# Performance work log

Measured on AMD Instinct MI355X. Metric: run time of the kernel, lower is better.

The kernel has to match this reference:

```python
import jax, jax.numpy as jnp
import numpy as np

FIRE_RATE = 0.5
ANGLE = 0.0

def _sobel_kernels(angle=ANGLE):
    dx = np.outer([1, 2, 1], [-1, 0, 1]) / 8.0
    dy = dx.T
    c = np.cos(angle * np.pi / 180.0)
    s = np.sin(angle * np.pi / 180.0)
    w1 = (c * dx - s * dy).astype(np.float32)
    w2 = (s * dx + c * dy).astype(np.float32)
    # torch applies conv after transpose(1,3) so its spatial axes are (W,H);
    # transposing kernels makes our NHWC conv over (H,W) match exactly.
    return jnp.asarray(w1.T), jnp.asarray(w2.T)

def _depthwise3x3(x, w):
    # x: [B,H,W,C], w: [3,3] shared across all C channels (groups=C)
    C = x.shape[-1]
    k = jnp.tile(w[:, :, None, None], (1, 1, 1, C))  # [3,3,1,C] HWIO
    return jax.lax.conv_general_dilated(
        x, k, window_strides=(1, 1), padding='SAME',
        dimension_numbers=('NHWC', 'HWIO', 'NHWC'),
        feature_group_count=C)

def setup_inputs() -> dict:
    key = jax.random.key(0)
    k1, k2, k3 = jax.random.split(key, 3)
    B, H, W, C, HID = 8, 256, 256, 16, 128
    x = jax.random.uniform(k1, (B, H, W, C), dtype=jnp.float32)
    # xavier-uniform-like init for fc0/fc1
    lim0 = float(np.sqrt(6.0 / (3 * C + HID)))
    lim1 = float(np.sqrt(6.0 / (HID + C)))
    W0 = jax.random.uniform(k2, (HID, 3 * C), minval=-lim0, maxval=lim0, dtype=jnp.float32)
    b0 = jnp.zeros((HID,), dtype=jnp.float32)
    W1 = jax.random.uniform(k3, (C, HID), minval=-lim1, maxval=lim1, dtype=jnp.float32)
    return {'x': x, 'W0': W0, 'b0': b0, 'W1': W1, 'steps': 2}

def reference(x, W0, b0, W1, steps):
    w1, w2 = _sobel_kernels()
    key = jax.random.key(42)
    for step in range(steps):
        # perceive: identity + two depthwise sobel filters -> [B,H,W,3C]
        y = jnp.concatenate([x, _depthwise3x3(x, w1), _depthwise3x3(x, w2)], axis=-1)
        # per-cell MLP
        h = jax.nn.relu(jnp.einsum('bhwk,ok->bhwo', y, W0) + b0)
        dx = jnp.einsum('bhwo,co->bhwc', h, W1)
        # stochastic fire-rate mask [B,H,W,1]
        mk = jax.random.fold_in(key, step)
        mask = (jax.random.uniform(mk, dx.shape[:3] + (1,)) > FIRE_RATE).astype(dx.dtype)
        new = x + dx * mask
        # only channels 3: are updated (first 3 channels stay fixed)
        x = jnp.concatenate([x[..., :3], new[..., 3:]], axis=-1)
    return x
```

## Files before the change

kernel.cpp:

```cpp
#include <hip/hip_runtime.h>
#include <hip/hip_bf16.h>
#include <stdint.h>


#define NB 8
#define NH 256
#define NW 256
#define NC 16
#define TH 4
#define TW 16
#define WOFF 65536

typedef __attribute__((ext_vector_type(8))) short short8;
typedef __attribute__((ext_vector_type(4))) float floatx4;

__host__ __device__ inline void tf2x32(uint32_t k0, uint32_t k1,
                                       uint32_t x0, uint32_t x1,
                                       uint32_t& o0, uint32_t& o1) {
  const uint32_t ks2 = k0 ^ k1 ^ 0x1BD11BDAu;
  x0 += k0; x1 += k1;
#define RL(v, d) (((v) << (d)) | ((v) >> (32 - (d))))
#define R4(a, b, c, d)                          \
  x0 += x1; x1 = RL(x1, a); x1 ^= x0;           \
  x0 += x1; x1 = RL(x1, b); x1 ^= x0;           \
  x0 += x1; x1 = RL(x1, c); x1 ^= x0;           \
  x0 += x1; x1 = RL(x1, d); x1 ^= x0;
  R4(13, 15, 26, 6);  x0 += k1;  x1 += ks2 + 1u;
  R4(17, 29, 16, 24); x0 += ks2; x1 += k0 + 2u;
  R4(13, 15, 26, 6);  x0 += k0;  x1 += k1 + 3u;
  R4(17, 29, 16, 24); x0 += k1;  x1 += ks2 + 4u;
  R4(13, 15, 26, 6);  x0 += ks2; x1 += k0 + 5u;
#undef R4
#undef RL
  o0 = x0; o1 = x1;
}

__device__ inline short bfr(float x) {
  __hip_bfloat16 h = __float2bfloat16(x);
  return *reinterpret_cast<short*>(&h);
}

__global__ __launch_bounds__(64) void ca_prep(
    const float* __restrict__ W0, const float* __restrict__ b0,
    const float* __restrict__ W1, short* __restrict__ wbuf) {
  const int lane = threadIdx.x;
  const int c15 = lane & 15;
  const int g = lane >> 4;
  short8* wf = reinterpret_cast<short8*>(wbuf);

#pragma unroll
  for (int n = 0; n < 8; ++n) {
    const int o = 16 * n + c15;
    const float* p = W0 + o * 48 + 8 * g;
    const floatx4 v0 = *reinterpret_cast<const floatx4*>(p);
    const floatx4 v1 = *reinterpret_cast<const floatx4*>(p + 4);
    short8 f;
    f[0] = bfr(v0.x); f[1] = bfr(v0.y); f[2] = bfr(v0.z); f[3] = bfr(v0.w);
    f[4] = bfr(v1.x); f[5] = bfr(v1.y); f[6] = bfr(v1.z); f[7] = bfr(v1.w);
    wf[(2 * n) * 64 + lane] = f;
    short8 f1;
    if (g < 2) {
      const float* p1 = W0 + o * 48 + 32 + 8 * g;
      const floatx4 u0 = *reinterpret_cast<const floatx4*>(p1);
      const floatx4 u1 = *reinterpret_cast<const floatx4*>(p1 + 4);
      f1[0] = bfr(u0.x); f1[1] = bfr(u0.y); f1[2] = bfr(u0.z); f1[3] = bfr(u0.w);
      f1[4] = bfr(u1.x); f1[5] = bfr(u1.y); f1[6] = bfr(u1.z); f1[7] = bfr(u1.w);
    } else {
#pragma unroll
      for (int j = 0; j < 8; ++j) f1[j] = 0;
      if (g == 2) f1[0] = bfr(b0[o]);
    }
    wf[(2 * n + 1) * 64 + lane] = f1;
  }
#pragma unroll
  for (int s = 0; s < 4; ++s) {
    const float* p = W1 + c15 * 128 + 32 * s + 4 * g;
    const floatx4 v0 = *reinterpret_cast<const floatx4*>(p);
    const floatx4 v1 = *reinterpret_cast<const floatx4*>(p + 16);
    short8 f;
    f[0] = bfr(v0.x); f[1] = bfr(v0.y); f[2] = bfr(v0.z); f[3] = bfr(v0.w);
    f[4] = bfr(v1.x); f[5] = bfr(v1.y); f[6] = bfr(v1.z); f[7] = bfr(v1.w);
    wf[(16 + s) * 64 + lane] = f;
  }
}

template <bool PRE>
__global__ __launch_bounds__(64, 2) void ca_step(
    const float* __restrict__ xin, float* __restrict__ xout,
    const float* __restrict__ W0, const float* __restrict__ b0,
    const float* __restrict__ W1, const short* __restrict__ wfrag,
    uint32_t fk0, uint32_t fk1) {
  __shared__ float xs[2][6 * 18 * 16];

  const int tid = threadIdx.x;
  const int bt = blockIdx.x;
  const int wt = bt & 15;
  const int ht8 = (bt >> 4) & 31;
  const int b = bt >> 9;
  const int h0 = ht8 * 8;
  const int w0 = wt * TW;

  const int lane = tid;
  const int c15 = lane & 15;
  const int g = lane >> 4;

  auto xsaddr = [&](float* base, int row, int col, int chunk) -> floatx4* {
    const int off = (row * 18 + col) * 64 + ((chunk ^ ((col >> 1) & 3)) << 4);
    return reinterpret_cast<floatx4*>(reinterpret_cast<char*>(base) + off);
  };

  short8 w0f[8][2];
  short8 w1f[4];
  if constexpr (PRE) {
    const short8* wf = reinterpret_cast<const short8*>(wfrag);
#pragma unroll
    for (int n = 0; n < 8; ++n) {
      w0f[n][0] = wf[(2 * n) * 64 + lane];
      w0f[n][1] = wf[(2 * n + 1) * 64 + lane];
    }
#pragma unroll
    for (int s = 0; s < 4; ++s) w1f[s] = wf[(16 + s) * 64 + lane];
  } else {
#pragma unroll
    for (int n = 0; n < 8; ++n) {
      const int o = 16 * n + c15;
      const float* p = W0 + o * 48 + 8 * g;
      const floatx4 v0 = *reinterpret_cast<const floatx4*>(p);
      const floatx4 v1 = *reinterpret_cast<const floatx4*>(p + 4);
      short8 f;
      f[0] = bfr(v0.x); f[1] = bfr(v0.y); f[2] = bfr(v0.z); f[3] = bfr(v0.w);
      f[4] = bfr(v1.x); f[5] = bfr(v1.y); f[6] = bfr(v1.z); f[7] = bfr(v1.w);
      w0f[n][0] = f;
      short8 f1;
      if (g < 2) {
        const float* p1 = W0 + o * 48 + 32 + 8 * g;
        const floatx4 u0 = *reinterpret_cast<const floatx4*>(p1);
        const floatx4 u1 = *reinterpret_cast<const floatx4*>(p1 + 4);
        f1[0] = bfr(u0.x); f1[1] = bfr(u0.y); f1[2] = bfr(u0.z); f1[3] = bfr(u0.w);
        f1[4] = bfr(u1.x); f1[5] = bfr(u1.y); f1[6] = bfr(u1.z); f1[7] = bfr(u1.w);
      } else {
#pragma unroll
        for (int j = 0; j < 8; ++j) f1[j] = 0;
        if (g == 2) f1[0] = bfr(b0[o]);
      }
      w0f[n][1] = f1;
    }
#pragma unroll
    for (int s = 0; s < 4; ++s) {
      const float* p = W1 + c15 * 128 + 32 * s + 4 * g;
      const floatx4 v0 = *reinterpret_cast<const floatx4*>(p);
      const floatx4 v1 = *reinterpret_cast<const floatx4*>(p + 16);
      short8 f;
      f[0] = bfr(v0.x); f[1] = bfr(v0.y); f[2] = bfr(v0.z); f[3] = bfr(v0.w);
      f[4] = bfr(v1.x); f[5] = bfr(v1.y); f[6] = bfr(v1.z); f[7] = bfr(v1.w);
      w1f[s] = f;
    }
  }

  float wts[8];
  {
    const float Ac[3] = {1.f, 2.f, 1.f};
    const float Bc[3] = {-1.f, 0.f, 1.f};
    int t = 0;
#pragma unroll
    for (int dh = -1; dh <= 1; ++dh)
#pragma unroll
      for (int dw = -1; dw <= 1; ++dw) {
        if (dh == 0 && dw == 0) continue;
        const float wA = Ac[dw + 1] * Bc[dh + 1] * 0.125f;
        const float wB = Ac[dh + 1] * Bc[dw + 1] * 0.125f;
        wts[t++] = (g < 2) ? wB : wA;
      }
  }

  const int cc = 2 * (g & 1);

#pragma unroll 1
  for (int t2 = 0; t2 < 2; ++t2) {
    const int h0t = h0 + TH * t2;
    float* xsb = xs[t2];

    for (int f = tid; f < 6 * 18 * 4; f += 64) {
      const int row = f / 72;
      const int rem = f - row * 72;
      const int col = rem >> 2;
      const int q = rem & 3;
      const int gh = h0t - 1 + row;
      const int gw = w0 - 1 + col;
      floatx4 v = {0.f, 0.f, 0.f, 0.f};
      if ((unsigned)gh < (unsigned)NH && (unsigned)gw < (unsigned)NW)
        v = *reinterpret_cast<const floatx4*>(
            xin + (((size_t)b * NH + gh) * NW + gw) * NC + 4 * q);
      *xsaddr(xsb, row, col, q) = v;
    }

    uint64_t mball;
    {
      const int cellg = (b * NH + h0t + (lane >> 4)) * NW + w0 + c15;
      uint32_t r0, r1;
      tf2x32(fk0, fk1, 0u, (uint32_t)cellg, r0, r1);
      const uint32_t bits = r0 ^ r1;
      const float u = __uint_as_float((bits >> 9) | 0x3F800000u) - 1.0f;
      mball = __ballot(u > 0.5f);
    }
    __syncthreads();

#pragma unroll
    for (int mt = 0; mt < 4; ++mt) {
      const int r = 1 + mt;
      const int col = 1 + c15;

      const floatx4 xc0 = *xsaddr(xsb, r, col, cc);
      const floatx4 xc1 = *xsaddr(xsb, r, col, cc + 1);

      float sob[8];
#pragma unroll
      for (int j = 0; j < 8; ++j) sob[j] = 0.f;
      int t = 0;
#pragma unroll
      for (int dh = -1; dh <= 1; ++dh)
#pragma unroll
        for (int dw = -1; dw <= 1; ++dw) {
          if (dh == 0 && dw == 0) continue;
          const floatx4 v0 = *xsaddr(xsb, r + dh, col + dw, cc);
          const floatx4 v1 = *xsaddr(xsb, r + dh, col + dw, cc + 1);
          const float w = wts[t++];
          sob[0] += w * v0.x; sob[1] += w * v0.y;
          sob[2] += w * v0.z; sob[3] += w * v0.w;
          sob[4] += w * v1.x; sob[5] += w * v1.y;
          sob[6] += w * v1.z; sob[7] += w * v1.w;
        }

      const bool lo = (g < 2);
      const float xcv[8] = {xc0.x, xc0.y, xc0.z, xc0.w,
                            xc1.x, xc1.y, xc1.z, xc1.w};
      short8 a0, a1;
#pragma unroll
      for (int j = 0; j < 8; ++j) {
        const short sb = bfr(sob[j]);
        a0[j] = lo ? bfr(xcv[j]) : sb;
        a1[j] = lo ? sb : (short)0;
      }
      if (g == 2) a1[0] = bfr(1.0f);

      floatx4 acc[8];
#pragma unroll
      for (int n = 0; n < 8; ++n) acc[n] = floatx4{0.f, 0.f, 0.f, 0.f};
#pragma unroll
      for (int n = 0; n < 8; ++n)
        acc[n] = __builtin_amdgcn_mfma_f32_16x16x32_bf16(w0f[n][0], a0, acc[n], 0, 0, 0);
#pragma unroll
      for (int n = 0; n < 8; ++n)
        acc[n] = __builtin_amdgcn_mfma_f32_16x16x32_bf16(w0f[n][1], a1, acc[n], 0, 0, 0);

      floatx4 acc2 = {0.f, 0.f, 0.f, 0.f};
#pragma unroll
      for (int s = 0; s < 4; ++s) {
        short8 b2;
#pragma unroll
        for (int j = 0; j < 8; ++j)
          b2[j] = bfr(fmaxf(acc[2 * s + (j >> 2)][j & 3], 0.f));
        acc2 = __builtin_amdgcn_mfma_f32_16x16x32_bf16(w1f[s], b2, acc2, 0, 0, 0);
      }

      const floatx4 xv = *xsaddr(xsb, r, col, g);
      const float mk = (float)((mball >> (16 * mt + c15)) & 1ull);
      const float mk03 = (g == 0) ? 0.f : mk;
      floatx4 ov;
      ov.x = xv.x + acc2.x * mk03;
      ov.y = xv.y + acc2.y * mk03;
      ov.z = xv.z + acc2.z * mk03;
      ov.w = xv.w + acc2.w * mk;
      const size_t cellg = ((size_t)(b * NH + h0t + mt)) * NW + w0 + c15;
      *reinterpret_cast<floatx4*>(xout + cellg * NC + 4 * g) = ov;
    }
  }
}

extern "C" void kernel_launch(void* const* d_in, const int* in_sizes, int n_in,
                              void* d_out, int out_size, void* d_ws, size_t ws_size,
                              hipStream_t stream) {
  const float* x  = (const float*)d_in[0];
  const float* W0 = (const float*)d_in[1];
  const float* b0 = (const float*)d_in[2];
  const float* W1 = (const float*)d_in[3];
  float* out = (float*)d_out;

  const size_t tmp_bytes = (size_t)NB * NH * NW * NC * 4;
  const bool pre = ws_size >= (size_t)WOFF + tmp_bytes;
  short* wbuf = (short*)d_ws;
  float* tmp = pre ? (float*)((char*)d_ws + WOFF) : (float*)d_ws;

  uint32_t fa0, fa1, fb0, fb1;
  tf2x32(0u, 42u, 0u, 0u, fa0, fa1);
  tf2x32(0u, 42u, 0u, 1u, fb0, fb1);

  dim3 grid(NB * (NH / 8) * (NW / TW)), block(64);
  if (pre) {
    ca_prep<<<1, 64, 0, stream>>>(W0, b0, W1, wbuf);
    ca_step<true><<<grid, block, 0, stream>>>(x, tmp, W0, b0, W1, wbuf, fa0, fa1);
    ca_step<true><<<grid, block, 0, stream>>>(tmp, out, W0, b0, W1, wbuf, fb0, fb1);
  } else {
    ca_step<false><<<grid, block, 0, stream>>>(x, tmp, W0, b0, W1, nullptr, fa0, fa1);
    ca_step<false><<<grid, block, 0, stream>>>(tmp, out, W0, b0, W1, nullptr, fb0, fb1);
  }
}
```

Before: 70.66 us.

## Fold Sobel stencil into first-layer weights and compute via im2col MFMA

Folds the two fixed Sobel filters and the identity into an expanded first-layer weight matrix over the 3x3 neighbourhood (K=144 plus a bias chunk), so the per-cell stencil FMAs become extra MFMA K-steps that read bf16 neighbours straight from shared memory. The shared tile now holds bf16 instead of fp32, which halves LDS use and drops to a single buffer with an extra barrier. The residual x is reread from global memory in fp32. In exchange, first-layer MFMAs go from 16 to 40 per tile, weight registers grow from 16 to 40 short8 fragments, and the Sobel sums are no longer done in fp32 before rounding, which changes the numerics.

After: 130.8 us. 85.1% more time.

```diff
diff --git a/kernel.cpp b/kernel.cpp
--- a/kernel.cpp
+++ b/kernel.cpp
@@ -7,8 +7,6 @@
 #define NH 256
 #define NW 256
 #define NC 16
-#define TH 4
-#define TW 16
 #define WOFF 65536
 
 typedef __attribute__((ext_vector_type(8))) short short8;
@@ -40,6 +38,20 @@
   return *reinterpret_cast<short*>(&h);
 }
 
+__device__ inline float w0comp(const float* __restrict__ W0,
+                               const float* __restrict__ b0, int o, int k) {
+  const int t = k >> 4;
+  const int ch = k & 15;
+  if (t == 9) return (ch == 0) ? b0[o] : 0.f;
+  const int dh = t / 3 - 1, dw = t % 3 - 1;
+  const float Ac[3] = {1.f, 2.f, 1.f};
+  const float Bc[3] = {-1.f, 0.f, 1.f};
+  float v = (t == 4) ? W0[o * 48 + ch] : 0.f;
+  v += Ac[dw + 1] * Bc[dh + 1] * 0.125f * W0[o * 48 + 16 + ch];
+  v += Ac[dh + 1] * Bc[dw + 1] * 0.125f * W0[o * 48 + 32 + ch];
+  return v;
+}
+
 __global__ __launch_bounds__(64) void ca_prep(
     const float* __restrict__ W0, const float* __restrict__ b0,
     const float* __restrict__ W1, short* __restrict__ wbuf) {
@@ -48,39 +60,22 @@
   const int g = lane >> 4;
   short8* wf = reinterpret_cast<short8*>(wbuf);
 
-#pragma unroll
-  for (int n = 0; n < 8; ++n) {
-    const int o = 16 * n + c15;
-    const float* p = W0 + o * 48 + 8 * g;
-    const floatx4 v0 = *reinterpret_cast<const floatx4*>(p);
-    const floatx4 v1 = *reinterpret_cast<const floatx4*>(p + 4);
+  for (int n = 0; n < 8; ++n)
+    for (int q = 0; q < 5; ++q) {
+      short8 f;
+#pragma unroll
+      for (int j = 0; j < 8; ++j)
+        f[j] = bfr(w0comp(W0, b0, 16 * n + c15, 32 * q + 8 * g + j));
+      wf[(n * 5 + q) * 64 + lane] = f;
+    }
+#pragma unroll
+  for (int s = 0; s < 4; ++s) {
+    const float* p = W1 + c15 * 128;
     short8 f;
-    f[0] = bfr(v0.x); f[1] = bfr(v0.y); f[2] = bfr(v0.z); f[3] = bfr(v0.w);
-    f[4] = bfr(v1.x); f[5] = bfr(v1.y); f[6] = bfr(v1.z); f[7] = bfr(v1.w);
-    wf[(2 * n) * 64 + lane] = f;
-    short8 f1;
-    if (g < 2) {
-      const float* p1 = W0 + o * 48 + 32 + 8 * g;
-      const floatx4 u0 = *reinterpret_cast<const floatx4*>(p1);
-      const floatx4 u1 = *reinterpret_cast<const floatx4*>(p1 + 4);
-      f1[0] = bfr(u0.x); f1[1] = bfr(u0.y); f1[2] = bfr(u0.z); f1[3] = bfr(u0.w);
-      f1[4] = bfr(u1.x); f1[5] = bfr(u1.y); f1[6] = bfr(u1.z); f1[7] = bfr(u1.w);
-    } else {
-#pragma unroll
-      for (int j = 0; j < 8; ++j) f1[j] = 0;
-      if (g == 2) f1[0] = bfr(b0[o]);
-    }
-    wf[(2 * n + 1) * 64 + lane] = f1;
-  }
-#pragma unroll
-  for (int s = 0; s < 4; ++s) {
-    const float* p = W1 + c15 * 128 + 32 * s + 4 * g;
-    const floatx4 v0 = *reinterpret_cast<const floatx4*>(p);
-    const floatx4 v1 = *reinterpret_cast<const floatx4*>(p + 16);
-    short8 f;
-    f[0] = bfr(v0.x); f[1] = bfr(v0.y); f[2] = bfr(v0.z); f[3] = bfr(v0.w);
-    f[4] = bfr(v1.x); f[5] = bfr(v1.y); f[6] = bfr(v1.z); f[7] = bfr(v1.w);
-    wf[(16 + s) * 64 + lane] = f;
+#pragma unroll
+    for (int j = 0; j < 8; ++j)
+      f[j] = bfr(p[32 * s + 16 * (j >> 2) + 4 * g + (j & 3)]);
+    wf[(40 + s) * 64 + lane] = f;
   }
 }
 
@@ -90,7 +85,7 @@
     const float* __restrict__ W0, const float* __restrict__ b0,
     const float* __restrict__ W1, const short* __restrict__ wfrag,
     uint32_t fk0, uint32_t fk1) {
-  __shared__ float xs[2][6 * 18 * 16];
+  __shared__ __align__(16) uint16_t xs[6 * 18 * 16];
 
   const int tid = threadIdx.x;
   const int bt = blockIdx.x;
@@ -98,100 +93,81 @@
   const int ht8 = (bt >> 4) & 31;
   const int b = bt >> 9;
   const int h0 = ht8 * 8;
-  const int w0 = wt * TW;
+  const int w0 = wt * 16;
 
   const int lane = tid;
   const int c15 = lane & 15;
   const int g = lane >> 4;
-
-  auto xsaddr = [&](float* base, int row, int col, int chunk) -> floatx4* {
-    const int off = (row * 18 + col) * 64 + ((chunk ^ ((col >> 1) & 3)) << 4);
-    return reinterpret_cast<floatx4*>(reinterpret_cast<char*>(base) + off);
-  };
-
-  short8 w0f[8][2];
+  const int hh0 = g & 1;
+  const int thalf = g >> 1;
+
+  short8 w0f[8][5];
   short8 w1f[4];
   if constexpr (PRE) {
     const short8* wf = reinterpret_cast<const short8*>(wfrag);
 #pragma unroll
-    for (int n = 0; n < 8; ++n) {
-      w0f[n][0] = wf[(2 * n) * 64 + lane];
-      w0f[n][1] = wf[(2 * n + 1) * 64 + lane];
-    }
-#pragma unroll
-    for (int s = 0; s < 4; ++s) w1f[s] = wf[(16 + s) * 64 + lane];
+    for (int n = 0; n < 8; ++n)
+#pragma unroll
+      for (int q = 0; q < 5; ++q) w0f[n][q] = wf[(n * 5 + q) * 64 + lane];
+#pragma unroll
+    for (int s = 0; s < 4; ++s) w1f[s] = wf[(40 + s) * 64 + lane];
   } else {
-#pragma unroll
-    for (int n = 0; n < 8; ++n) {
-      const int o = 16 * n + c15;
-      const float* p = W0 + o * 48 + 8 * g;
-      const floatx4 v0 = *reinterpret_cast<const floatx4*>(p);
-      const floatx4 v1 = *reinterpret_cast<const floatx4*>(p + 4);
+    for (int n = 0; n < 8; ++n)
+      for (int q = 0; q < 5; ++q) {
+        short8 f;
+#pragma unroll
+        for (int j = 0; j < 8; ++j)
+          f[j] = bfr(w0comp(W0, b0, 16 * n + c15, 32 * q + 8 * g + j));
+        w0f[n][q] = f;
+      }
+#pragma unroll
+    for (int s = 0; s < 4; ++s) {
+      const float* p = W1 + c15 * 128;
       short8 f;
-      f[0] = bfr(v0.x); f[1] = bfr(v0.y); f[2] = bfr(v0.z); f[3] = bfr(v0.w);
-      f[4] = bfr(v1.x); f[5] = bfr(v1.y); f[6] = bfr(v1.z); f[7] = bfr(v1.w);
-      w0f[n][0] = f;
-      short8 f1;
-      if (g < 2) {
-        const float* p1 = W0 + o * 48 + 32 + 8 * g;
-        const floatx4 u0 = *reinterpret_cast<const floatx4*>(p1);
-        const floatx4 u1 = *reinterpret_cast<const floatx4*>(p1 + 4);
-        f1[0] = bfr(u0.x); f1[1] = bfr(u0.y); f1[2] = bfr(u0.z); f1[3] = bfr(u0.w);
-        f1[4] = bfr(u1.x); f1[5] = bfr(u1.y); f1[6] = bfr(u1.z); f1[7] = bfr(u1.w);
-      } else {
-#pragma unroll
-        for (int j = 0; j < 8; ++j) f1[j] = 0;
-        if (g == 2) f1[0] = bfr(b0[o]);
-      }
-      w0f[n][1] = f1;
-    }
-#pragma unroll
-    for (int s = 0; s < 4; ++s) {
-      const float* p = W1 + c15 * 128 + 32 * s + 4 * g;
-      const floatx4 v0 = *reinterpret_cast<const floatx4*>(p);
-      const floatx4 v1 = *reinterpret_cast<const floatx4*>(p + 16);
-      short8 f;
-      f[0] = bfr(v0.x); f[1] = bfr(v0.y); f[2] = bfr(v0.z); f[3] = bfr(v0.w);
-      f[4] = bfr(v1.x); f[5] = bfr(v1.y); f[6] = bfr(v1.z); f[7] = bfr(v1.w);
+#pragma unroll
+      for (int j = 0; j < 8; ++j)
+        f[j] = bfr(p[32 * s + 16 * (j >> 2) + 4 * g + (j & 3)]);
       w1f[s] = f;
     }
   }
 
-  float wts[8];
-  {
-    const float Ac[3] = {1.f, 2.f, 1.f};
-    const float Bc[3] = {-1.f, 0.f, 1.f};
-    int t = 0;
-#pragma unroll
-    for (int dh = -1; dh <= 1; ++dh)
-#pragma unroll
-      for (int dw = -1; dw <= 1; ++dw) {
-        if (dh == 0 && dw == 0) continue;
-        const float wA = Ac[dw + 1] * Bc[dh + 1] * 0.125f;
-        const float wB = Ac[dh + 1] * Bc[dw + 1] * 0.125f;
-        wts[t++] = (g < 2) ? wB : wA;
-      }
-  }
-
-  const int cc = 2 * (g & 1);
+  int doff[5];
+#pragma unroll
+  for (int q = 0; q < 5; ++q) {
+    int t = 2 * q + thalf;
+    if (t > 8) t = 8;
+    const int dh = t / 3 - 1, dw = t % 3 - 1;
+    doff[q] = (dh * 18 + dw) * 16;
+  }
+  short8 cb;
+#pragma unroll
+  for (int j = 0; j < 8; ++j) cb[j] = 0;
+  if (g == 2) cb[0] = bfr(1.0f);
 
 #pragma unroll 1
   for (int t2 = 0; t2 < 2; ++t2) {
-    const int h0t = h0 + TH * t2;
-    float* xsb = xs[t2];
-
-    for (int f = tid; f < 6 * 18 * 4; f += 64) {
-      const int row = f / 72;
-      const int rem = f - row * 72;
-      const int col = rem >> 2;
-      const int q = rem & 3;
+    const int h0t = h0 + 4 * t2;
+
+    __syncthreads();
+
+    for (int f = tid; f < 216; f += 64) {
+      const int row = f / 36;
+      const int rem = f - row * 36;
+      const int col = rem >> 1;
+      const int hx = rem & 1;
       const int gh = h0t - 1 + row;
       const int gw = w0 - 1 + col;
-      floatx4 v = {0.f, 0.f, 0.f, 0.f};
-      if ((unsigned)gh < (unsigned)NH && (unsigned)gw < (unsigned)NW)
-        v = *reinterpret_cast<const floatx4*>(
-            xin + (((size_t)b * NH + gh) * NW + gw) * NC + 4 * q);
-      *xsaddr(xsb, row, col, q) = v;
+      short8 v;
+#pragma unroll
+      for (int j = 0; j < 8; ++j) v[j] = 0;
+      if ((unsigned)gh < (unsigned)NH && (unsigned)gw < (unsigned)NW) {
+        const float* p = xin + (((size_t)b * NH + gh) * NW + gw) * NC + 8 * hx;
+        const floatx4 u0 = *reinterpret_cast<const floatx4*>(p);
+        const floatx4 u1 = *reinterpret_cast<const floatx4*>(p + 4);
+        v[0] = bfr(u0.x); v[1] = bfr(u0.y); v[2] = bfr(u0.z); v[3] = bfr(u0.w);
+        v[4] = bfr(u1.x); v[5] = bfr(u1.y); v[6] = bfr(u1.z); v[7] = bfr(u1.w);
+      }
+      *reinterpret_cast<short8*>(&xs[(row * 18 + col) * 16 + hx * 8]) = v;
     }
 
     uint64_t mball;
@@ -207,51 +183,27 @@
 
 #pragma unroll
     for (int mt = 0; mt < 4; ++mt) {
-      const int r = 1 + mt;
-      const int col = 1 + c15;
-
-      const floatx4 xc0 = *xsaddr(xsb, r, col, cc);
-      const floatx4 xc1 = *xsaddr(xsb, r, col, cc + 1);
-
-      float sob[8];
-#pragma unroll
-      for (int j = 0; j < 8; ++j) sob[j] = 0.f;
-      int t = 0;
-#pragma unroll
-      for (int dh = -1; dh <= 1; ++dh)
-#pragma unroll
-        for (int dw = -1; dw <= 1; ++dw) {
-          if (dh == 0 && dw == 0) continue;
-          const floatx4 v0 = *xsaddr(xsb, r + dh, col + dw, cc);
-          const floatx4 v1 = *xsaddr(xsb, r + dh, col + dw, cc + 1);
-          const float w = wts[t++];
-          sob[0] += w * v0.x; sob[1] += w * v0.y;
-          sob[2] += w * v0.z; sob[3] += w * v0.w;
-          sob[4] += w * v1.x; sob[5] += w * v1.y;
-          sob[6] += w * v1.z; sob[7] += w * v1.w;
-        }
-
-      const bool lo = (g < 2);
-      const float xcv[8] = {xc0.x, xc0.y, xc0.z, xc0.w,
-                            xc1.x, xc1.y, xc1.z, xc1.w};
-      short8 a0, a1;
-#pragma unroll
-      for (int j = 0; j < 8; ++j) {
-        const short sb = bfr(sob[j]);
-        a0[j] = lo ? bfr(xcv[j]) : sb;
-        a1[j] = lo ? sb : (short)0;
-      }
-      if (g == 2) a1[0] = bfr(1.0f);
+      const int cidx = ((1 + mt) * 18 + 1 + c15) * 16 + hh0 * 8;
+
+      const size_t cellg = ((size_t)(b * NH + h0t + mt)) * NW + w0 + c15;
+      const floatx4 xv =
+          *reinterpret_cast<const floatx4*>(xin + cellg * NC + 4 * g);
+
+      short8 bq[5];
+#pragma unroll
+      for (int q = 0; q < 5; ++q)
+        bq[q] = *reinterpret_cast<const short8*>(&xs[cidx + doff[q]]);
+      if (g >= 2) bq[4] = cb;
 
       floatx4 acc[8];
 #pragma unroll
       for (int n = 0; n < 8; ++n) acc[n] = floatx4{0.f, 0.f, 0.f, 0.f};
 #pragma unroll
-      for (int n = 0; n < 8; ++n)
-        acc[n] = __builtin_amdgcn_mfma_f32_16x16x32_bf16(w0f[n][0], a0, acc[n], 0, 0, 0);
-#pragma unroll
-      for (int n = 0; n < 8; ++n)
-        acc[n] = __builtin_amdgcn_mfma_f32_16x16x32_bf16(w0f[n][1], a1, acc[n], 0, 0, 0);
+      for (int q = 0; q < 5; ++q)
+#pragma unroll
+        for (int n = 0; n < 8; ++n)
+          acc[n] =
+              __builtin_amdgcn_mfma_f32_16x16x32_bf16(w0f[n][q], bq[q], acc[n], 0, 0, 0);
 
       floatx4 acc2 = {0.f, 0.f, 0.f, 0.f};
 #pragma unroll
@@ -263,7 +215,6 @@
         acc2 = __builtin_amdgcn_mfma_f32_16x16x32_bf16(w1f[s], b2, acc2, 0, 0, 0);
       }
 
-      const floatx4 xv = *xsaddr(xsb, r, col, g);
       const float mk = (float)((mball >> (16 * mt + c15)) & 1ull);
       const float mk03 = (g == 0) ? 0.f : mk;
       floatx4 ov;
@@ -271,7 +222,6 @@
       ov.y = xv.y + acc2.y * mk03;
       ov.z = xv.z + acc2.z * mk03;
       ov.w = xv.w + acc2.w * mk;
-      const size_t cellg = ((size_t)(b * NH + h0t + mt)) * NW + w0 + c15;
       *reinterpret_cast<floatx4*>(xout + cellg * NC + 4 * g) = ov;
     }
   }
@@ -295,7 +245,7 @@
   tf2x32(0u, 42u, 0u, 0u, fa0, fa1);
   tf2x32(0u, 42u, 0u, 1u, fb0, fb1);
 
-  dim3 grid(NB * (NH / 8) * (NW / TW)), block(64);
+  dim3 grid(NB * (NH / 8) * (NW / 16)), block(64);
   if (pre) {
     ca_prep<<<1, 64, 0, stream>>>(W0, b0, W1, wbuf);
     ca_step<true><<<grid, block, 0, stream>>>(x, tmp, W0, b0, W1, wbuf, fa0, fa1);
```
